# Kernel optimization log

Hardware: AMD Instinct MI355X
Metric: run time of the kernel (lower is better)

## Reference

```python
import jax, jax.numpy as jnp
import numpy as np

K = 7            # kernel_size
PAD = (K - 1) // 2
C = 64           # channels
GC = 4           # group_channels (hardcoded in module)
G = C // GC      # groups = 16
CR = C // 2      # reduction_ratio = 2
EPS = 1e-5


def setup_inputs() -> dict:
    key = jax.random.key(0)
    ks = jax.random.split(key, 8)
    b, h, w = 4, 128, 128
    x = jax.random.normal(ks[0], (b, C, h, w), dtype=jnp.float32)
    y = jax.random.normal(ks[1], (b, C, h, w), dtype=jnp.float32)
    # conv1: 1x1 conv C -> C//2, plus BatchNorm (eval-style) params
    w1 = jax.random.normal(ks[2], (CR, C), dtype=jnp.float32) * (1.0 / np.sqrt(C))
    b1 = jnp.zeros((CR,), dtype=jnp.float32)
    bn_gamma = jnp.ones((CR,), dtype=jnp.float32)
    bn_beta = jnp.zeros((CR,), dtype=jnp.float32)
    bn_mean = jax.random.normal(ks[3], (CR,), dtype=jnp.float32) * 0.1
    bn_var = jax.random.uniform(ks[4], (CR,), dtype=jnp.float32, minval=0.5, maxval=1.5)
    # conv2: 1x1 conv C//2 -> K^2 * groups
    w2 = jax.random.normal(ks[5], (K * K * G, CR), dtype=jnp.float32) * (1.0 / np.sqrt(CR))
    b2 = jnp.zeros((K * K * G,), dtype=jnp.float32)
    return {"x": x, "y": y, "w1": w1, "b1": b1, "bn_gamma": bn_gamma,
            "bn_beta": bn_beta, "bn_mean": bn_mean, "bn_var": bn_var,
            "w2": w2, "b2": b2}


def _unfold_patches(y):
    # y: (b, C, h, w) -> (b, C, K*K, h, w) im2col with zero padding PAD, stride 1
    b, c, h, w = y.shape
    yp = jnp.pad(y, ((0, 0), (0, 0), (PAD, PAD), (PAD, PAD)))
    # fixed K*K loop over kernel offsets (structural, not data-dim loop)
    patches = jnp.stack([yp[:, :, i:i + h, j:j + w]
                         for i in range(K) for j in range(K)], axis=2)
    return patches  # (b, C, K^2, h, w)


def reference(x, y, w1, b1, bn_gamma, bn_beta, bn_mean, bn_var, w2, b2):
    b, c, h, w = x.shape
    # conv1: 1x1 conv + BN(eval) + ReLU
    t = jnp.einsum('oc,bchw->bohw', w1, x) + b1[None, :, None, None]
    inv_std = jax.lax.rsqrt(bn_var + EPS)
    t = (t - bn_mean[None, :, None, None]) * (bn_gamma * inv_std)[None, :, None, None] \
        + bn_beta[None, :, None, None]
    t = jax.nn.relu(t)
    # conv2: 1x1 conv -> per-pixel kernels, (b, G, K^2, h, w)
    weight = jnp.einsum('oc,bchw->bohw', w2, t) + b2[None, :, None, None]
    weight = weight.reshape(b, G, K * K, h, w)
    # unfold y -> (b, G, GC, K^2, h, w)
    patches = _unfold_patches(y).reshape(b, G, GC, K * K, h, w)
    # dynamic depthwise aggregation: sum over K^2
    out = jnp.einsum('bgkhw,bgckhw->bgchw', weight, patches)
    return out.reshape(b, C, h, w)
```

## Files before the change

### kernel.cpp

```cpp
#include <hip/hip_runtime.h>

#define K7   7
#define PAD3 3
#define C64  64
#define CRED 32
#define GC4  4
#define EPSV 1e-5f

#define TILE 8
#define HALO 14
#define NPIX (HALO * HALO)

typedef _Float16 half8 __attribute__((ext_vector_type(8)));
typedef _Float16 half4 __attribute__((ext_vector_type(4)));
typedef float    f32x4 __attribute__((ext_vector_type(4)));

__global__ __launch_bounds__(256, 4)
void conv1_bn_relu(const float* __restrict__ x,  const float* __restrict__ w1,
                   const float* __restrict__ b1, const float* __restrict__ gma,
                   const float* __restrict__ bta, const float* __restrict__ mu,
                   const float* __restrict__ var, _Float16* __restrict__ t)
{
    const int tid = threadIdx.x;
    const int p   = tid & 63;
    const int oq  = __builtin_amdgcn_readfirstlane(tid >> 6);
    const int task = blockIdx.x * 64 + p;
    const int b   = task >> 14;
    const int pix = task & 16383;

    float dot[8] = {0,0,0,0,0,0,0,0};
    const float* w1q = w1 + oq * 8 * C64;
    const float* xp  = x + ((size_t)b << 20) + pix;
    #pragma unroll 8
    for (int c = 0; c < C64; ++c) {
        float xc = xp[(size_t)c << 14];
        #pragma unroll
        for (int j = 0; j < 8; ++j) dot[j] += w1q[j * C64 + c] * xc;
    }
    _Float16 tv[8];
    #pragma unroll
    for (int j = 0; j < 8; ++j) {
        int o = oq * 8 + j;
        float sv = gma[o] * rsqrtf(var[o] + EPSV);
        float bb = (b1[o] - mu[o]) * sv + bta[o];
        tv[j] = (_Float16)fmaxf(dot[j] * sv + bb, 0.f);
    }
    *(half8*)&t[((size_t)((b << 14) + pix)) * 32 + oq * 8] = *(const half8*)tv;
}

#define NCH2 16
#define NSL2 4
#define YPS  20
#define W2ST 40
#define W2G  (49 * W2ST)

__global__ __launch_bounds__(256, 4)
void invol_agg(const float* __restrict__ y, const _Float16* __restrict__ t,
               const float* __restrict__ w2, const float* __restrict__ b2,
               float* __restrict__ out)
{
    __shared__ __align__(16) _Float16 ytile[NPIX * YPS];
    __shared__ __align__(16) _Float16 w2h[NSL2 * W2G];

    const int tid = threadIdx.x;
    const int wgid = blockIdx.x + (blockIdx.y << 4) + (blockIdx.z << 8);
    const int swz  = ((wgid & 7) << 9) | (wgid >> 3);
    const int bx = swz & 15, by = (swz >> 4) & 15, bz = swz >> 8;
    const int b = bz >> 2, quarter = bz & 3;
    const int gh0 = by * TILE, gw0 = bx * TILE;
    const int c0 = quarter * NCH2;

    const int p  = tid & 63;
    const int ph = p >> 3, pw = p & 7;
    const int oq = __builtin_amdgcn_readfirstlane(tid >> 6);
    const int q  = p >> 4, r = p & 15;
    const int pix = ((gh0 + ph) << 7) + (gw0 + pw);

    const _Float16* tb = t + ((size_t)(b << 14)) * 32;
    const int rr8 = r >> 3, rc = r & 7;
    half8 bfrag0 = *(const half8*)&tb[(size_t)(((gh0 + 0 + rr8) << 7) + gw0 + rc) * 32 + q * 8];
    half8 bfrag1 = *(const half8*)&tb[(size_t)(((gh0 + 2 + rr8) << 7) + gw0 + rc) * 32 + q * 8];
    half8 bfrag2 = *(const half8*)&tb[(size_t)(((gh0 + 4 + rr8) << 7) + gw0 + rc) * 32 + q * 8];
    half8 bfrag3 = *(const half8*)&tb[(size_t)(((gh0 + 6 + rr8) << 7) + gw0 + rc) * 32 + q * 8];

    for (int u = tid; u < 4 * NPIX; u += 256) {
        int cg   = u / NPIX;
        int pixl = u - cg * NPIX;
        int rr   = pixl / HALO;
        int col  = pixl - rr * HALO;
        int grow = gh0 - PAD3 + rr;
        int gcol = gw0 - PAD3 + col;
        half4 v = {(_Float16)0.f, (_Float16)0.f, (_Float16)0.f, (_Float16)0.f};
        if ((unsigned)grow < 128u && (unsigned)gcol < 128u) {
            const float* yp = y + ((size_t)(b * C64 + c0 + cg * 4) << 14) + (grow << 7) + gcol;
            v[0] = (_Float16)yp[0];
            v[1] = (_Float16)yp[1 << 14];
            v[2] = (_Float16)yp[2 << 14];
            v[3] = (_Float16)yp[3 << 14];
        }
        *(half4*)&ytile[pixl * YPS + cg * 4] = v;
    }

    for (int u = tid; u < NSL2 * 49 * 8; u += 256) {
        int lg  = u / 392;
        int rem = u - lg * 392;
        int row = rem >> 3;
        int k4  = (rem & 7) << 2;
        const float4 w4 = *(const float4*)&w2[(((quarter * NSL2 + lg) * 49 + row) << 5) + k4];
        half4 h;
        h[0] = (_Float16)w4.x; h[1] = (_Float16)w4.y;
        h[2] = (_Float16)w4.z; h[3] = (_Float16)w4.w;
        *(half4*)&w2h[lg * W2G + row * W2ST + k4] = h;
    }
    __syncthreads();

    const int pbF0 = ((0 + rr8) * HALO + rc) * YPS + oq * 4;
    const int pbF1 = ((2 + rr8) * HALO + rc) * YPS + oq * 4;
    const int pbF2 = ((4 + rr8) * HALO + rc) * YPS + oq * 4;
    const int pbF3 = ((6 + rr8) * HALO + rc) * YPS + oq * 4;

    const f32x4 zero = {0.f, 0.f, 0.f, 0.f};

    const int g  = quarter * NSL2 + oq;
    const float* b2g = b2 + g * 49;
    const _Float16* w2hg = w2h + oq * W2G;

    float acc[4][4];
    #pragma unroll
    for (int nt = 0; nt < 4; ++nt)
        #pragma unroll
        for (int c = 0; c < 4; ++c) acc[nt][c] = 0.f;

    #pragma clang loop unroll(disable)
    for (int mt = 0; mt < 3; ++mt) {
        const half8 af = *(const half8*)&w2hg[(mt * 16 + r) * W2ST + q * 8];
        const int bi = mt * 16 + q * 4;
        const f32x4 cb = { b2g[bi+0], b2g[bi+1], b2g[bi+2], b2g[bi+3] };

        f32x4 d0 = __builtin_amdgcn_mfma_f32_16x16x32_f16(af, bfrag0, cb, 0, 0, 0);
        f32x4 d1 = __builtin_amdgcn_mfma_f32_16x16x32_f16(af, bfrag1, cb, 0, 0, 0);
        f32x4 d2 = __builtin_amdgcn_mfma_f32_16x16x32_f16(af, bfrag2, cb, 0, 0, 0);
        f32x4 d3 = __builtin_amdgcn_mfma_f32_16x16x32_f16(af, bfrag3, cb, 0, 0, 0);

        #pragma unroll
        for (int reg = 0; reg < 4; ++reg) {
            const int tap = mt * 16 + q * 4 + reg;
            const int di = (tap * 9363) >> 16;
            const int toffF = (tap + 7 * di) * YPS;
            {
                const float wv = d0[reg];
                const half4 y4 = *(const half4*)&ytile[pbF0 + toffF];
                acc[0][0] += (float)y4[0] * wv; acc[0][1] += (float)y4[1] * wv;
                acc[0][2] += (float)y4[2] * wv; acc[0][3] += (float)y4[3] * wv;
            }
            {
                const float wv = d1[reg];
                const half4 y4 = *(const half4*)&ytile[pbF1 + toffF];
                acc[1][0] += (float)y4[0] * wv; acc[1][1] += (float)y4[1] * wv;
                acc[1][2] += (float)y4[2] * wv; acc[1][3] += (float)y4[3] * wv;
            }
            {
                const float wv = d2[reg];
                const half4 y4 = *(const half4*)&ytile[pbF2 + toffF];
                acc[2][0] += (float)y4[0] * wv; acc[2][1] += (float)y4[1] * wv;
                acc[2][2] += (float)y4[2] * wv; acc[2][3] += (float)y4[3] * wv;
            }
            {
                const float wv = d3[reg];
                const half4 y4 = *(const half4*)&ytile[pbF3 + toffF];
                acc[3][0] += (float)y4[0] * wv; acc[3][1] += (float)y4[1] * wv;
                acc[3][2] += (float)y4[2] * wv; acc[3][3] += (float)y4[3] * wv;
            }
        }
    }

    {
        half8 af = *(const half8*)&w2hg[48 * W2ST + q * 8];
        if (r != 0) {
            #pragma unroll
            for (int j = 0; j < 8; ++j) af[j] = (_Float16)0.f;
        }
        f32x4 d0 = __builtin_amdgcn_mfma_f32_16x16x32_f16(af, bfrag0, zero, 0, 0, 0);
        f32x4 d1 = __builtin_amdgcn_mfma_f32_16x16x32_f16(af, bfrag1, zero, 0, 0, 0);
        f32x4 d2 = __builtin_amdgcn_mfma_f32_16x16x32_f16(af, bfrag2, zero, 0, 0, 0);
        f32x4 d3 = __builtin_amdgcn_mfma_f32_16x16x32_f16(af, bfrag3, zero, 0, 0, 0);

        const float bv = b2g[48];
        const int toffF = (48 + 7 * 6) * YPS;
        const bool live = (q == 0);
        {
            float wv = live ? (d0[0] + bv) : 0.f;
            const half4 y4 = *(const half4*)&ytile[pbF0 + toffF];
            acc[0][0] += (float)y4[0] * wv; acc[0][1] += (float)y4[1] * wv;
            acc[0][2] += (float)y4[2] * wv; acc[0][3] += (float)y4[3] * wv;
        }
        {
            float wv = live ? (d1[0] + bv) : 0.f;
            const half4 y4 = *(const half4*)&ytile[pbF1 + toffF];
            acc[1][0] += (float)y4[0] * wv; acc[1][1] += (float)y4[1] * wv;
            acc[1][2] += (float)y4[2] * wv; acc[1][3] += (float)y4[3] * wv;
        }
        {
            float wv = live ? (d2[0] + bv) : 0.f;
            const half4 y4 = *(const half4*)&ytile[pbF2 + toffF];
            acc[2][0] += (float)y4[0] * wv; acc[2][1] += (float)y4[1] * wv;
            acc[2][2] += (float)y4[2] * wv; acc[2][3] += (float)y4[3] * wv;
        }
        {
            float wv = live ? (d3[0] + bv) : 0.f;
            const half4 y4 = *(const half4*)&ytile[pbF3 + toffF];
            acc[3][0] += (float)y4[0] * wv; acc[3][1] += (float)y4[1] * wv;
            acc[3][2] += (float)y4[2] * wv; acc[3][3] += (float)y4[3] * wv;
        }
    }

    #pragma unroll
    for (int nt = 0; nt < 4; ++nt)
        #pragma unroll
        for (int c = 0; c < 4; ++c) {
            float v = acc[nt][c];
            v += __shfl_xor(v, 16);
            v += __shfl_xor(v, 32);
            acc[nt][c] = v;
        }

    size_t ob = ((size_t)(b * C64 + g * GC4) << 14) + pix;
    #pragma unroll
    for (int c = 0; c < 4; ++c) {
        float s0 = (q & 1) ? acc[1][c] : acc[0][c];
        float s1 = (q & 1) ? acc[3][c] : acc[2][c];
        float vv = (q & 2) ? s1 : s0;
        out[ob + ((size_t)c << 14)] = vv;
    }
}

#define NCHF 32
#define NSLF 8
#define TSTH 40

__global__ __launch_bounds__(256, 2)
void involution_fused_fb(const float* __restrict__ x, const float* __restrict__ y,
                         const float* __restrict__ w1, const float* __restrict__ b1,
                         const float* __restrict__ gma, const float* __restrict__ bta,
                         const float* __restrict__ mu,  const float* __restrict__ var,
                         const float* __restrict__ w2,  const float* __restrict__ b2,
                         float* __restrict__ out)
{
    __shared__ __align__(16) float    ytile[NPIX * NCHF];
    __shared__ __align__(16) _Float16 t_lds[64 * TSTH];

    const int tid = threadIdx.x;
    const int bx = blockIdx.x, by = blockIdx.y, bz = blockIdx.z;
    const int b = bz >> 1, half = bz & 1;
    const int gh0 = by * TILE, gw0 = bx * TILE;
    const int c0 = half * NCHF;

    for (int li = tid; li < NCHF * NPIX; li += 256) {
        int c    = li / NPIX;
        int pixl = li - c * NPIX;
        int rr   = pixl / HALO;
        int col  = pixl - rr * HALO;
        int grow = gh0 - PAD3 + rr;
        int gcol = gw0 - PAD3 + col;
        float v = 0.f;
        if ((unsigned)grow < 128u && (unsigned)gcol < 128u)
            v = y[((size_t)(b * C64 + c0 + c) << 14) + (grow << 7) + gcol];
        int slot = ((c >> 2) + pixl) & 7;
        ytile[pixl * NCHF + slot * 4 + (c & 3)] = v;
    }

    const int p  = tid & 63;
    const int ph = p >> 3, pw = p & 7;
    const int oq = __builtin_amdgcn_readfirstlane(tid >> 6);
    const int pix = ((gh0 + ph) << 7) + (gw0 + pw);
    {
        float dot[8] = {0,0,0,0,0,0,0,0};
        const float* w1q = w1 + oq * 8 * C64;
        const float* xp  = x + ((size_t)(b * C64) << 14) + pix;
        #pragma unroll 8
        for (int c = 0; c < C64; ++c) {
            float xc = xp[(size_t)c << 14];
            #pragma unroll
            for (int j = 0; j < 8; ++j) dot[j] += w1q[j * C64 + c] * xc;
        }
        _Float16 tv16[8];
        #pragma unroll
        for (int j = 0; j < 8; ++j) {
            int o = oq * 8 + j;
            float sv = gma[o] * rsqrtf(var[o] + EPSV);
            float bb = (b1[o] - mu[o]) * sv + bta[o];
            tv16[j] = (_Float16)fmaxf(dot[j] * sv + bb, 0.f);
        }
        *(half8*)&t_lds[p * TSTH + oq * 8] = *(const half8*)tv16;
    }
    __syncthreads();

    const int q = p >> 4;
    const int r = p & 15;

    half8 bfrag0 = *(const half8*)&t_lds[( 0 + r) * TSTH + q * 8];
    half8 bfrag1 = *(const half8*)&t_lds[(16 + r) * TSTH + q * 8];
    half8 bfrag2 = *(const half8*)&t_lds[(32 + r) * TSTH + q * 8];
    half8 bfrag3 = *(const half8*)&t_lds[(48 + r) * TSTH + q * 8];

    const int pb0 = (0 + (r >> 3)) * HALO + (r & 7);
    const int pb1 = (2 + (r >> 3)) * HALO + (r & 7);
    const int pb2 = (4 + (r >> 3)) * HALO + (r & 7);
    const int pb3 = (6 + (r >> 3)) * HALO + (r & 7);

    const f32x4 zero = {0.f, 0.f, 0.f, 0.f};

    #pragma unroll 1
    for (int lgi = 0; lgi < 2; ++lgi) {
        const int lg = oq * 2 + lgi;
        const int g  = half * NSLF + lg;
        const float* w2g = w2 + g * 49 * CRED;
        const float* b2g = b2 + g * 49;

        float acc[4][4];
        #pragma unroll
        for (int nt = 0; nt < 4; ++nt)
            #pragma unroll
            for (int c = 0; c < 4; ++c) acc[nt][c] = 0.f;

        #pragma clang loop unroll(disable)
        for (int mt = 0; mt < 3; ++mt) {
            half8 af;
            {
                const float* wr = w2g + (mt * 16 + r) * CRED + q * 8;
                float4 wa = *(const float4*)wr;
                float4 wb = *(const float4*)(wr + 4);
                af[0] = (_Float16)wa.x; af[1] = (_Float16)wa.y;
                af[2] = (_Float16)wa.z; af[3] = (_Float16)wa.w;
                af[4] = (_Float16)wb.x; af[5] = (_Float16)wb.y;
                af[6] = (_Float16)wb.z; af[7] = (_Float16)wb.w;
            }
            f32x4 d0 = __builtin_amdgcn_mfma_f32_16x16x32_f16(af, bfrag0, zero, 0, 0, 0);
            f32x4 d1 = __builtin_amdgcn_mfma_f32_16x16x32_f16(af, bfrag1, zero, 0, 0, 0);
            f32x4 d2 = __builtin_amdgcn_mfma_f32_16x16x32_f16(af, bfrag2, zero, 0, 0, 0);
            f32x4 d3 = __builtin_amdgcn_mfma_f32_16x16x32_f16(af, bfrag3, zero, 0, 0, 0);

            #pragma unroll
            for (int reg = 0; reg < 4; ++reg) {
                const int tap = mt * 16 + q * 4 + reg;
                const float bv = b2g[tap];
                const int di = (tap * 9363) >> 16;
                const int tapoff = tap + 7 * di;
                {
                    float wv = d0[reg] + bv;
                    int tp2 = pb0 + tapoff;
                    const float4 y4 = *(const float4*)&ytile[tp2 * NCHF + (((lg + tp2) & 7) << 2)];
                    acc[0][0] += wv * y4.x; acc[0][1] += wv * y4.y;
                    acc[0][2] += wv * y4.z; acc[0][3] += wv * y4.w;
                }
                {
                    float wv = d1[reg] + bv;
                    int tp2 = pb1 + tapoff;
                    const float4 y4 = *(const float4*)&ytile[tp2 * NCHF + (((lg + tp2) & 7) << 2)];
                    acc[1][0] += wv * y4.x; acc[1][1] += wv * y4.y;
                    acc[1][2] += wv * y4.z; acc[1][3] += wv * y4.w;
                }
                {
                    float wv = d2[reg] + bv;
                    int tp2 = pb2 + tapoff;
                    const float4 y4 = *(const float4*)&ytile[tp2 * NCHF + (((lg + tp2) & 7) << 2)];
                    acc[2][0] += wv * y4.x; acc[2][1] += wv * y4.y;
                    acc[2][2] += wv * y4.z; acc[2][3] += wv * y4.w;
                }
                {
                    float wv = d3[reg] + bv;
                    int tp2 = pb3 + tapoff;
                    const float4 y4 = *(const float4*)&ytile[tp2 * NCHF + (((lg + tp2) & 7) << 2)];
                    acc[3][0] += wv * y4.x; acc[3][1] += wv * y4.y;
                    acc[3][2] += wv * y4.z; acc[3][3] += wv * y4.w;
                }
            }
        }

        {
            half8 af;
            #pragma unroll
            for (int j = 0; j < 8; ++j) af[j] = (_Float16)0.f;
            if (r == 0) {
                const float* wr = w2g + 48 * CRED + q * 8;
                float4 wa = *(const float4*)wr;
                float4 wb = *(const float4*)(wr + 4);
                af[0] = (_Float16)wa.x; af[1] = (_Float16)wa.y;
                af[2] = (_Float16)wa.z; af[3] = (_Float16)wa.w;
                af[4] = (_Float16)wb.x; af[5] = (_Float16)wb.y;
                af[6] = (_Float16)wb.z; af[7] = (_Float16)wb.w;
            }
            f32x4 d0 = __builtin_amdgcn_mfma_f32_16x16x32_f16(af, bfrag0, zero, 0, 0, 0);
            f32x4 d1 = __builtin_amdgcn_mfma_f32_16x16x32_f16(af, bfrag1, zero, 0, 0, 0);
            f32x4 d2 = __builtin_amdgcn_mfma_f32_16x16x32_f16(af, bfrag2, zero, 0, 0, 0);
            f32x4 d3 = __builtin_amdgcn_mfma_f32_16x16x32_f16(af, bfrag3, zero, 0, 0, 0);

            const float bv = b2g[48];
            const int tapoff = 48 + 7 * 6;
            const bool live = (q == 0);
            {
                float wv = live ? (d0[0] + bv) : 0.f;
                int tp2 = pb0 + tapoff;
                const float4 y4 = *(const float4*)&ytile[tp2 * NCHF + (((lg + tp2) & 7) << 2)];
                acc[0][0] += wv * y4.x; acc[0][1] += wv * y4.y;
                acc[0][2] += wv * y4.z; acc[0][3] += wv * y4.w;
            }
            {
                float wv = live ? (d1[0] + bv) : 0.f;
                int tp2 = pb1 + tapoff;
                const float4 y4 = *(const float4*)&ytile[tp2 * NCHF + (((lg + tp2) & 7) << 2)];
                acc[1][0] += wv * y4.x; acc[1][1] += wv * y4.y;
                acc[1][2] += wv * y4.z; acc[1][3] += wv * y4.w;
            }
            {
                float wv = live ? (d2[0] + bv) : 0.f;
                int tp2 = pb2 + tapoff;
                const float4 y4 = *(const float4*)&ytile[tp2 * NCHF + (((lg + tp2) & 7) << 2)];
                acc[2][0] += wv * y4.x; acc[2][1] += wv * y4.y;
                acc[2][2] += wv * y4.z; acc[2][3] += wv * y4.w;
            }
            {
                float wv = live ? (d3[0] + bv) : 0.f;
                int tp2 = pb3 + tapoff;
                const float4 y4 = *(const float4*)&ytile[tp2 * NCHF + (((lg + tp2) & 7) << 2)];
                acc[3][0] += wv * y4.x; acc[3][1] += wv * y4.y;
                acc[3][2] += wv * y4.z; acc[3][3] += wv * y4.w;
            }
        }

        #pragma unroll
        for (int nt = 0; nt < 4; ++nt)
            #pragma unroll
            for (int c = 0; c < 4; ++c) {
                float v = acc[nt][c];
                v += __shfl_xor(v, 16);
                v += __shfl_xor(v, 32);
                acc[nt][c] = v;
            }

        size_t ob = ((size_t)(b * C64 + g * GC4) << 14) + pix;
        #pragma unroll
        for (int c = 0; c < 4; ++c) {
            float s0 = (q & 1) ? acc[1][c] : acc[0][c];
            float s1 = (q & 1) ? acc[3][c] : acc[2][c];
            float vv = (q & 2) ? s1 : s0;
            out[ob + ((size_t)c << 14)] = vv;
        }
    }
}

extern "C" void kernel_launch(void* const* d_in, const int* in_sizes, int n_in,
                              void* d_out, int out_size, void* d_ws, size_t ws_size,
                              hipStream_t stream) {
    const float* x   = (const float*)d_in[0];
    const float* y   = (const float*)d_in[1];
    const float* w1  = (const float*)d_in[2];
    const float* b1  = (const float*)d_in[3];
    const float* gma = (const float*)d_in[4];
    const float* bta = (const float*)d_in[5];
    const float* mu  = (const float*)d_in[6];
    const float* var = (const float*)d_in[7];
    const float* w2  = (const float*)d_in[8];
    const float* b2  = (const float*)d_in[9];
    float* out = (float*)d_out;

    const size_t t_bytes = (size_t)4 * 16384 * 32 * sizeof(_Float16);
    if (ws_size >= t_bytes) {
        _Float16* t = (_Float16*)d_ws;
        hipLaunchKernelGGL(conv1_bn_relu, dim3(1024), dim3(256), 0, stream,
                           x, w1, b1, gma, bta, mu, var, t);
        hipLaunchKernelGGL(invol_agg, dim3(16, 16, 16), dim3(256), 0, stream,
                           y, t, w2, b2, out);
    } else {
        hipLaunchKernelGGL(involution_fused_fb, dim3(16, 16, 8), dim3(256), 0, stream,
                           x, y, w1, b1, gma, bta, mu, var, w2, b2, out);
    }
}
```

Before: 45.70 us.

## Process two groups per wave in involution aggregation to halve tile loads

```diff
diff --git a/kernel.cpp b/kernel.cpp
--- a/kernel.cpp
+++ b/kernel.cpp
@@ -48,27 +48,26 @@
     *(half8*)&t[((size_t)((b << 14) + pix)) * 32 + oq * 8] = *(const half8*)tv;
 }
 
-#define NCH2 16
-#define NSL2 4
-#define YPS  20
+#define NSLH 8
+#define YPS  40
 #define W2ST 40
 #define W2G  (49 * W2ST)
 
-__global__ __launch_bounds__(256, 4)
+__global__ __launch_bounds__(256, 2)
 void invol_agg(const float* __restrict__ y, const _Float16* __restrict__ t,
                const float* __restrict__ w2, const float* __restrict__ b2,
                float* __restrict__ out)
 {
     __shared__ __align__(16) _Float16 ytile[NPIX * YPS];
-    __shared__ __align__(16) _Float16 w2h[NSL2 * W2G];
+    __shared__ __align__(16) _Float16 w2h[NSLH * W2G];
 
     const int tid = threadIdx.x;
     const int wgid = blockIdx.x + (blockIdx.y << 4) + (blockIdx.z << 8);
-    const int swz  = ((wgid & 7) << 9) | (wgid >> 3);
+    const int swz  = ((wgid & 7) << 8) | (wgid >> 3);
     const int bx = swz & 15, by = (swz >> 4) & 15, bz = swz >> 8;
-    const int b = bz >> 2, quarter = bz & 3;
+    const int b = bz >> 1, half = bz & 1;
     const int gh0 = by * TILE, gw0 = bx * TILE;
-    const int c0 = quarter * NCH2;
+    const int c0 = half * 32;
 
     const int p  = tid & 63;
     const int ph = p >> 3, pw = p & 7;
@@ -83,7 +82,7 @@
     half8 bfrag2 = *(const half8*)&tb[(size_t)(((gh0 + 4 + rr8) << 7) + gw0 + rc) * 32 + q * 8];
     half8 bfrag3 = *(const half8*)&tb[(size_t)(((gh0 + 6 + rr8) << 7) + gw0 + rc) * 32 + q * 8];
 
-    for (int u = tid; u < 4 * NPIX; u += 256) {
+    for (int u = tid; u < 8 * NPIX; u += 256) {
         int cg   = u / NPIX;
         int pixl = u - cg * NPIX;
         int rr   = pixl / HALO;
@@ -101,12 +100,12 @@
         *(half4*)&ytile[pixl * YPS + cg * 4] = v;
     }
 
-    for (int u = tid; u < NSL2 * 49 * 8; u += 256) {
+    for (int u = tid; u < NSLH * 49 * 8; u += 256) {
         int lg  = u / 392;
         int rem = u - lg * 392;
         int row = rem >> 3;
         int k4  = (rem & 7) << 2;
-        const float4 w4 = *(const float4*)&w2[(((quarter * NSL2 + lg) * 49 + row) << 5) + k4];
+        const float4 w4 = *(const float4*)&w2[(((half * NSLH + lg) * 49 + row) << 5) + k4];
         half4 h;
         h[0] = (_Float16)w4.x; h[1] = (_Float16)w4.y;
         h[2] = (_Float16)w4.z; h[3] = (_Float16)w4.w;
@@ -114,33 +113,42 @@
     }
     __syncthreads();
 
-    const int pbF0 = ((0 + rr8) * HALO + rc) * YPS + oq * 4;
-    const int pbF1 = ((2 + rr8) * HALO + rc) * YPS + oq * 4;
-    const int pbF2 = ((4 + rr8) * HALO + rc) * YPS + oq * 4;
-    const int pbF3 = ((6 + rr8) * HALO + rc) * YPS + oq * 4;
+    const int pbF0 = ((0 + rr8) * HALO + rc) * YPS + oq * 8;
+    const int pbF1 = ((2 + rr8) * HALO + rc) * YPS + oq * 8;
+    const int pbF2 = ((4 + rr8) * HALO + rc) * YPS + oq * 8;
+    const int pbF3 = ((6 + rr8) * HALO + rc) * YPS + oq * 8;
 
     const f32x4 zero = {0.f, 0.f, 0.f, 0.f};
 
-    const int g  = quarter * NSL2 + oq;
-    const float* b2g = b2 + g * 49;
-    const _Float16* w2hg = w2h + oq * W2G;
-
-    float acc[4][4];
+    const int lg0 = 2 * oq, lg1 = 2 * oq + 1;
+    const int g0  = half * NSLH + lg0;
+    const float* b2g0 = b2 + g0 * 49;
+    const float* b2g1 = b2 + (g0 + 1) * 49;
+    const _Float16* w2hg0 = w2h + lg0 * W2G;
+    const _Float16* w2hg1 = w2h + lg1 * W2G;
+
+    float acc0[4][4], acc1[4][4];
     #pragma unroll
     for (int nt = 0; nt < 4; ++nt)
         #pragma unroll
-        for (int c = 0; c < 4; ++c) acc[nt][c] = 0.f;
+        for (int c = 0; c < 4; ++c) { acc0[nt][c] = 0.f; acc1[nt][c] = 0.f; }
 
     #pragma clang loop unroll(disable)
     for (int mt = 0; mt < 3; ++mt) {
-        const half8 af = *(const half8*)&w2hg[(mt * 16 + r) * W2ST + q * 8];
+        const half8 af0 = *(const half8*)&w2hg0[(mt * 16 + r) * W2ST + q * 8];
+        const half8 af1 = *(const half8*)&w2hg1[(mt * 16 + r) * W2ST + q * 8];
         const int bi = mt * 16 + q * 4;
-        const f32x4 cb = { b2g[bi+0], b2g[bi+1], b2g[bi+2], b2g[bi+3] };
-
-        f32x4 d0 = __builtin_amdgcn_mfma_f32_16x16x32_f16(af, bfrag0, cb, 0, 0, 0);
-        f32x4 d1 = __builtin_amdgcn_mfma_f32_16x16x32_f16(af, bfrag1, cb, 0, 0, 0);
-        f32x4 d2 = __builtin_amdgcn_mfma_f32_16x16x32_f16(af, bfrag2, cb, 0, 0, 0);
-        f32x4 d3 = __builtin_amdgcn_mfma_f32_16x16x32_f16(af, bfrag3, cb, 0, 0, 0);
+        const f32x4 cb0 = { b2g0[bi+0], b2g0[bi+1], b2g0[bi+2], b2g0[bi+3] };
+        const f32x4 cb1 = { b2g1[bi+0], b2g1[bi+1], b2g1[bi+2], b2g1[bi+3] };
+
+        f32x4 d0 = __builtin_amdgcn_mfma_f32_16x16x32_f16(af0, bfrag0, cb0, 0, 0, 0);
+        f32x4 d1 = __builtin_amdgcn_mfma_f32_16x16x32_f16(af0, bfrag1, cb0, 0, 0, 0);
+        f32x4 d2 = __builtin_amdgcn_mfma_f32_16x16x32_f16(af0, bfrag2, cb0, 0, 0, 0);
+        f32x4 d3 = __builtin_amdgcn_mfma_f32_16x16x32_f16(af0, bfrag3, cb0, 0, 0, 0);
+        f32x4 e0 = __builtin_amdgcn_mfma_f32_16x16x32_f16(af1, bfrag0, cb1, 0, 0, 0);
+        f32x4 e1 = __builtin_amdgcn_mfma_f32_16x16x32_f16(af1, bfrag1, cb1, 0, 0, 0);
+        f32x4 e2 = __builtin_amdgcn_mfma_f32_16x16x32_f16(af1, bfrag2, cb1, 0, 0, 0);
+        f32x4 e3 = __builtin_amdgcn_mfma_f32_16x16x32_f16(af1, bfrag3, cb1, 0, 0, 0);
 
         #pragma unroll
         for (int reg = 0; reg < 4; ++reg) {
@@ -148,69 +156,94 @@
             const int di = (tap * 9363) >> 16;
             const int toffF = (tap + 7 * di) * YPS;
             {
-                const float wv = d0[reg];
-                const half4 y4 = *(const half4*)&ytile[pbF0 + toffF];
-                acc[0][0] += (float)y4[0] * wv; acc[0][1] += (float)y4[1] * wv;
-                acc[0][2] += (float)y4[2] * wv; acc[0][3] += (float)y4[3] * wv;
-            }
-            {
-                const float wv = d1[reg];
-                const half4 y4 = *(const half4*)&ytile[pbF1 + toffF];
-                acc[1][0] += (float)y4[0] * wv; acc[1][1] += (float)y4[1] * wv;
-                acc[1][2] += (float)y4[2] * wv; acc[1][3] += (float)y4[3] * wv;
-            }
-            {
-                const float wv = d2[reg];
-                const half4 y4 = *(const half4*)&ytile[pbF2 + toffF];
-                acc[2][0] += (float)y4[0] * wv; acc[2][1] += (float)y4[1] * wv;
-                acc[2][2] += (float)y4[2] * wv; acc[2][3] += (float)y4[3] * wv;
-            }
-            {
-                const float wv = d3[reg];
-                const half4 y4 = *(const half4*)&ytile[pbF3 + toffF];
-                acc[3][0] += (float)y4[0] * wv; acc[3][1] += (float)y4[1] * wv;
-                acc[3][2] += (float)y4[2] * wv; acc[3][3] += (float)y4[3] * wv;
+                const half8 y8 = *(const half8*)&ytile[pbF0 + toffF];
+                const float wv = d0[reg], ev = e0[reg];
+                acc0[0][0] += (float)y8[0] * wv; acc0[0][1] += (float)y8[1] * wv;
+                acc0[0][2] += (float)y8[2] * wv; acc0[0][3] += (float)y8[3] * wv;
+                acc1[0][0] += (float)y8[4] * ev; acc1[0][1] += (float)y8[5] * ev;
+                acc1[0][2] += (float)y8[6] * ev; acc1[0][3] += (float)y8[7] * ev;
+            }
+            {
+                const half8 y8 = *(const half8*)&ytile[pbF1 + toffF];
+                const float wv = d1[reg], ev = e1[reg];
+                acc0[1][0] += (float)y8[0] * wv; acc0[1][1] += (float)y8[1] * wv;
+                acc0[1][2] += (float)y8[2] * wv; acc0[1][3] += (float)y8[3] * wv;
+                acc1[1][0] += (float)y8[4] * ev; acc1[1][1] += (float)y8[5] * ev;
+                acc1[1][2] += (float)y8[6] * ev; acc1[1][3] += (float)y8[7] * ev;
+            }
+            {
+                const half8 y8 = *(const half8*)&ytile[pbF2 + toffF];
+                const float wv = d2[reg], ev = e2[reg];
+                acc0[2][0] += (float)y8[0] * wv; acc0[2][1] += (float)y8[1] * wv;
+                acc0[2][2] += (float)y8[2] * wv; acc0[2][3] += (float)y8[3] * wv;
+                acc1[2][0] += (float)y8[4] * ev; acc1[2][1] += (float)y8[5] * ev;
+                acc1[2][2] += (float)y8[6] * ev; acc1[2][3] += (float)y8[7] * ev;
+            }
+            {
+                const half8 y8 = *(const half8*)&ytile[pbF3 + toffF];
+                const float wv = d3[reg], ev = e3[reg];
+                acc0[3][0] += (float)y8[0] * wv; acc0[3][1] += (float)y8[1] * wv;
+                acc0[3][2] += (float)y8[2] * wv; acc0[3][3] += (float)y8[3] * wv;
+                acc1[3][0] += (float)y8[4] * ev; acc1[3][1] += (float)y8[5] * ev;
+                acc1[3][2] += (float)y8[6] * ev; acc1[3][3] += (float)y8[7] * ev;
             }
         }
     }
 
     {
-        half8 af = *(const half8*)&w2hg[48 * W2ST + q * 8];
+        half8 af0 = *(const half8*)&w2hg0[48 * W2ST + q * 8];
+        half8 af1 = *(const half8*)&w2hg1[48 * W2ST + q * 8];
         if (r != 0) {
             #pragma unroll
-            for (int j = 0; j < 8; ++j) af[j] = (_Float16)0.f;
-        }
-        f32x4 d0 = __builtin_amdgcn_mfma_f32_16x16x32_f16(af, bfrag0, zero, 0, 0, 0);
-        f32x4 d1 = __builtin_amdgcn_mfma_f32_16x16x32_f16(af, bfrag1, zero, 0, 0, 0);
-        f32x4 d2 = __builtin_amdgcn_mfma_f32_16x16x32_f16(af, bfrag2, zero, 0, 0, 0);
-        f32x4 d3 = __builtin_amdgcn_mfma_f32_16x16x32_f16(af, bfrag3, zero, 0, 0, 0);
-
-        const float bv = b2g[48];
+            for (int j = 0; j < 8; ++j) { af0[j] = (_Float16)0.f; af1[j] = (_Float16)0.f; }
+        }
+        f32x4 d0 = __builtin_amdgcn_mfma_f32_16x16x32_f16(af0, bfrag0, zero, 0, 0, 0);
+        f32x4 d1 = __builtin_amdgcn_mfma_f32_16x16x32_f16(af0, bfrag1, zero, 0, 0, 0);
+        f32x4 d2 = __builtin_amdgcn_mfma_f32_16x16x32_f16(af0, bfrag2, zero, 0, 0, 0);
+        f32x4 d3 = __builtin_amdgcn_mfma_f32_16x16x32_f16(af0, bfrag3, zero, 0, 0, 0);
+        f32x4 e0 = __builtin_amdgcn_mfma_f32_16x16x32_f16(af1, bfrag0, zero, 0, 0, 0);
+        f32x4 e1 = __builtin_amdgcn_mfma_f32_16x16x32_f16(af1, bfrag1, zero, 0, 0, 0);
+        f32x4 e2 = __builtin_amdgcn_mfma_f32_16x16x32_f16(af1, bfrag2, zero, 0, 0, 0);
+        f32x4 e3 = __builtin_amdgcn_mfma_f32_16x16x32_f16(af1, bfrag3, zero, 0, 0, 0);
+
+        const float bv0 = b2g0[48], bv1 = b2g1[48];
         const int toffF = (48 + 7 * 6) * YPS;
         const bool live = (q == 0);
         {
-            float wv = live ? (d0[0] + bv) : 0.f;
-            const half4 y4 = *(const half4*)&ytile[pbF0 + toffF];
-            acc[0][0] += (float)y4[0] * wv; acc[0][1] += (float)y4[1] * wv;
-            acc[0][2] += (float)y4[2] * wv; acc[0][3] += (float)y4[3] * wv;
+            const half8 y8 = *(const half8*)&ytile[pbF0 + toffF];
+            float wv = live ? (d0[0] + bv0) : 0.f;
+            float ev = live ? (e0[0] + bv1) : 0.f;
+            acc0[0][0] += (float)y8[0] * wv; acc0[0][1] += (float)y8[1] * wv;
+            acc0[0][2] += (float)y8[2] * wv; acc0[0][3] += (float)y8[3] * wv;
+            acc1[0][0] += (float)y8[4] * ev; acc1[0][1] += (float)y8[5] * ev;
+            acc1[0][2] += (float)y8[6] * ev; acc1[0][3] += (float)y8[7] * ev;
         }
         {
-            float wv = live ? (d1[0] + bv) : 0.f;
-            const half4 y4 = *(const half4*)&ytile[pbF1 + toffF];
-            acc[1][0] += (float)y4[0] * wv; acc[1][1] += (float)y4[1] * wv;
-            acc[1][2] += (float)y4[2] * wv; acc[1][3] += (float)y4[3] * wv;
+            const half8 y8 = *(const half8*)&ytile[pbF1 + toffF];
+            float wv = live ? (d1[0] + bv0) : 0.f;
+            float ev = live ? (e1[0] + bv1) : 0.f;
+            acc0[1][0] += (float)y8[0] * wv; acc0[1][1] += (float)y8[1] * wv;
+            acc0[1][2] += (float)y8[2] * wv; acc0[1][3] += (float)y8[3] * wv;
+            acc1[1][0] += (float)y8[4] * ev; acc1[1][1] += (float)y8[5] * ev;
+            acc1[1][2] += (float)y8[6] * ev; acc1[1][3] += (float)y8[7] * ev;
         }
         {
-            float wv = live ? (d2[0] + bv) : 0.f;
-            const half4 y4 = *(const half4*)&ytile[pbF2 + toffF];
-            acc[2][0] += (float)y4[0] * wv; acc[2][1] += (float)y4[1] * wv;
-            acc[2][2] += (float)y4[2] * wv; acc[2][3] += (float)y4[3] * wv;
+            const half8 y8 = *(const half8*)&ytile[pbF2 + toffF];
+            float wv = live ? (d2[0] + bv0) : 0.f;
+            float ev = live ? (e2[0] + bv1) : 0.f;
+            acc0[2][0] += (float)y8[0] * wv; acc0[2][1] += (float)y8[1] * wv;
+            acc0[2][2] += (float)y8[2] * wv; acc0[2][3] += (float)y8[3] * wv;
+            acc1[2][0] += (float)y8[4] * ev; acc1[2][1] += (float)y8[5] * ev;
+            acc1[2][2] += (float)y8[6] * ev; acc1[2][3] += (float)y8[7] * ev;
         }
         {
-            float wv = live ? (d3[0] + bv) : 0.f;
-            const half4 y4 = *(const half4*)&ytile[pbF3 + toffF];
-            acc[3][0] += (float)y4[0] * wv; acc[3][1] += (float)y4[1] * wv;
-            acc[3][2] += (float)y4[2] * wv; acc[3][3] += (float)y4[3] * wv;
+            const half8 y8 = *(const half8*)&ytile[pbF3 + toffF];
+            float wv = live ? (d3[0] + bv0) : 0.f;
+            float ev = live ? (e3[0] + bv1) : 0.f;
+            acc0[3][0] += (float)y8[0] * wv; acc0[3][1] += (float)y8[1] * wv;
+            acc0[3][2] += (float)y8[2] * wv; acc0[3][3] += (float)y8[3] * wv;
+            acc1[3][0] += (float)y8[4] * ev; acc1[3][1] += (float)y8[5] * ev;
+            acc1[3][2] += (float)y8[6] * ev; acc1[3][3] += (float)y8[7] * ev;
         }
     }
 
@@ -218,19 +251,28 @@
     for (int nt = 0; nt < 4; ++nt)
         #pragma unroll
         for (int c = 0; c < 4; ++c) {
-            float v = acc[nt][c];
-            v += __shfl_xor(v, 16);
-            v += __shfl_xor(v, 32);
-            acc[nt][c] = v;
-        }
-
-    size_t ob = ((size_t)(b * C64 + g * GC4) << 14) + pix;
+            float v0 = acc0[nt][c];
+            v0 += __shfl_xor(v0, 16);
+            v0 += __shfl_xor(v0, 32);
+            acc0[nt][c] = v0;
+            float v1 = acc1[nt][c];
+            v1 += __shfl_xor(v1, 16);
+            v1 += __shfl_xor(v1, 32);
+            acc1[nt][c] = v1;
+        }
+
+    size_t ob = ((size_t)(b * C64 + g0 * GC4) << 14) + pix;
     #pragma unroll
     for (int c = 0; c < 4; ++c) {
-        float s0 = (q & 1) ? acc[1][c] : acc[0][c];
-        float s1 = (q & 1) ? acc[3][c] : acc[2][c];
-        float vv = (q & 2) ? s1 : s0;
-        out[ob + ((size_t)c << 14)] = vv;
+        float s0 = (q & 1) ? acc0[1][c] : acc0[0][c];
+        float s1 = (q & 1) ? acc0[3][c] : acc0[2][c];
+        out[ob + ((size_t)c << 14)] = (q & 2) ? s1 : s0;
+    }
+    #pragma unroll
+    for (int c = 0; c < 4; ++c) {
+        float s0 = (q & 1) ? acc1[1][c] : acc1[0][c];
+        float s1 = (q & 1) ? acc1[3][c] : acc1[2][c];
+        out[ob + ((size_t)(c + 4) << 14)] = (q & 2) ? s1 : s0;
     }
 }
 
@@ -469,7 +511,7 @@
         _Float16* t = (_Float16*)d_ws;
         hipLaunchKernelGGL(conv1_bn_relu, dim3(1024), dim3(256), 0, stream,
                            x, w1, b1, gma, bta, mu, var, t);
-        hipLaunchKernelGGL(invol_agg, dim3(16, 16, 16), dim3(256), 0, stream,
+        hipLaunchKernelGGL(invol_agg, dim3(16, 16, 8), dim3(256), 0, stream,
                            y, t, w2, b2, out);
     } else {
         hipLaunchKernelGGL(involution_fused_fb, dim3(16, 16, 8), dim3(256), 0, stream,
```

After: 48.37 us. 5.9% more time.

## Widen aggregation tile to 8x16 pixels with eight MFMA column blocks

Applied to the files above, without the earlier changes.

```diff
diff --git a/kernel.cpp b/kernel.cpp
--- a/kernel.cpp
+++ b/kernel.cpp
@@ -6,10 +6,6 @@
 #define CRED 32
 #define GC4  4
 #define EPSV 1e-5f
-
-#define TILE 8
-#define HALO 14
-#define NPIX (HALO * HALO)
 
 typedef _Float16 half8 __attribute__((ext_vector_type(8)));
 typedef _Float16 half4 __attribute__((ext_vector_type(4)));
@@ -48,46 +44,51 @@
     *(half8*)&t[((size_t)((b << 14) + pix)) * 32 + oq * 8] = *(const half8*)tv;
 }
 
-#define NCH2 16
+#define TH   8
+#define TW   16
+#define HH2  14
+#define HW2  22
+#define NPIX2 (HH2 * HW2)
 #define NSL2 4
 #define YPS  20
 #define W2ST 40
 #define W2G  (49 * W2ST)
 
-__global__ __launch_bounds__(256, 4)
+__global__ __launch_bounds__(256, 2)
 void invol_agg(const float* __restrict__ y, const _Float16* __restrict__ t,
                const float* __restrict__ w2, const float* __restrict__ b2,
                float* __restrict__ out)
 {
-    __shared__ __align__(16) _Float16 ytile[NPIX * YPS];
+    __shared__ __align__(16) _Float16 ytile[NPIX2 * YPS];
     __shared__ __align__(16) _Float16 w2h[NSL2 * W2G];
 
     const int tid = threadIdx.x;
-    const int wgid = blockIdx.x + (blockIdx.y << 4) + (blockIdx.z << 8);
-    const int swz  = ((wgid & 7) << 9) | (wgid >> 3);
-    const int bx = swz & 15, by = (swz >> 4) & 15, bz = swz >> 8;
+    const int wgid = blockIdx.x + (blockIdx.y << 3) + (blockIdx.z << 7);
+    const int swz  = ((wgid & 7) << 8) | (wgid >> 3);
+    const int bx = swz & 7, by = (swz >> 3) & 15, bz = swz >> 7;
     const int b = bz >> 2, quarter = bz & 3;
-    const int gh0 = by * TILE, gw0 = bx * TILE;
-    const int c0 = quarter * NCH2;
+    const int gh0 = by * TH, gw0 = bx * TW;
+    const int c0 = quarter * 16;
 
     const int p  = tid & 63;
-    const int ph = p >> 3, pw = p & 7;
     const int oq = __builtin_amdgcn_readfirstlane(tid >> 6);
     const int q  = p >> 4, r = p & 15;
-    const int pix = ((gh0 + ph) << 7) + (gw0 + pw);
 
     const _Float16* tb = t + ((size_t)(b << 14)) * 32;
-    const int rr8 = r >> 3, rc = r & 7;
-    half8 bfrag0 = *(const half8*)&tb[(size_t)(((gh0 + 0 + rr8) << 7) + gw0 + rc) * 32 + q * 8];
-    half8 bfrag1 = *(const half8*)&tb[(size_t)(((gh0 + 2 + rr8) << 7) + gw0 + rc) * 32 + q * 8];
-    half8 bfrag2 = *(const half8*)&tb[(size_t)(((gh0 + 4 + rr8) << 7) + gw0 + rc) * 32 + q * 8];
-    half8 bfrag3 = *(const half8*)&tb[(size_t)(((gh0 + 6 + rr8) << 7) + gw0 + rc) * 32 + q * 8];
-
-    for (int u = tid; u < 4 * NPIX; u += 256) {
-        int cg   = u / NPIX;
-        int pixl = u - cg * NPIX;
-        int rr   = pixl / HALO;
-        int col  = pixl - rr * HALO;
+    half8 bf0 = *(const half8*)&tb[(size_t)(((gh0 + 0) << 7) + gw0 + r) * 32 + q * 8];
+    half8 bf1 = *(const half8*)&tb[(size_t)(((gh0 + 1) << 7) + gw0 + r) * 32 + q * 8];
+    half8 bf2 = *(const half8*)&tb[(size_t)(((gh0 + 2) << 7) + gw0 + r) * 32 + q * 8];
+    half8 bf3 = *(const half8*)&tb[(size_t)(((gh0 + 3) << 7) + gw0 + r) * 32 + q * 8];
+    half8 bf4 = *(const half8*)&tb[(size_t)(((gh0 + 4) << 7) + gw0 + r) * 32 + q * 8];
+    half8 bf5 = *(const half8*)&tb[(size_t)(((gh0 + 5) << 7) + gw0 + r) * 32 + q * 8];
+    half8 bf6 = *(const half8*)&tb[(size_t)(((gh0 + 6) << 7) + gw0 + r) * 32 + q * 8];
+    half8 bf7 = *(const half8*)&tb[(size_t)(((gh0 + 7) << 7) + gw0 + r) * 32 + q * 8];
+
+    for (int u = tid; u < 4 * NPIX2; u += 256) {
+        int cg   = u / NPIX2;
+        int pixl = u - cg * NPIX2;
+        int rr   = pixl / HW2;
+        int col  = pixl - rr * HW2;
         int grow = gh0 - PAD3 + rr;
         int gcol = gw0 - PAD3 + col;
         half4 v = {(_Float16)0.f, (_Float16)0.f, (_Float16)0.f, (_Float16)0.f};
@@ -114,22 +115,40 @@
     }
     __syncthreads();
 
-    const int pbF0 = ((0 + rr8) * HALO + rc) * YPS + oq * 4;
-    const int pbF1 = ((2 + rr8) * HALO + rc) * YPS + oq * 4;
-    const int pbF2 = ((4 + rr8) * HALO + rc) * YPS + oq * 4;
-    const int pbF3 = ((6 + rr8) * HALO + rc) * YPS + oq * 4;
+    const int pbF0 = (0 * HW2 + r) * YPS + oq * 4;
+    const int pbF1 = (1 * HW2 + r) * YPS + oq * 4;
+    const int pbF2 = (2 * HW2 + r) * YPS + oq * 4;
+    const int pbF3 = (3 * HW2 + r) * YPS + oq * 4;
+    const int pbF4 = (4 * HW2 + r) * YPS + oq * 4;
+    const int pbF5 = (5 * HW2 + r) * YPS + oq * 4;
+    const int pbF6 = (6 * HW2 + r) * YPS + oq * 4;
+    const int pbF7 = (7 * HW2 + r) * YPS + oq * 4;
 
     const f32x4 zero = {0.f, 0.f, 0.f, 0.f};
 
-    const int g  = quarter * NSL2 + oq;
+    const int g = quarter * NSL2 + oq;
     const float* b2g = b2 + g * 49;
     const _Float16* w2hg = w2h + oq * W2G;
 
-    float acc[4][4];
+    float acc[8][4];
     #pragma unroll
-    for (int nt = 0; nt < 4; ++nt)
+    for (int nt = 0; nt < 8; ++nt)
         #pragma unroll
         for (int c = 0; c < 4; ++c) acc[nt][c] = 0.f;
+
+#define AGG(NT, DV) do { \
+        const half4 y4 = *(const half4*)&ytile[pbF##NT + toffF]; \
+        const float wv = (DV)[reg]; \
+        acc[NT][0] += (float)y4[0] * wv; acc[NT][1] += (float)y4[1] * wv; \
+        acc[NT][2] += (float)y4[2] * wv; acc[NT][3] += (float)y4[3] * wv; \
+    } while (0)
+
+#define AGGT(NT, DV) do { \
+        const half4 y4 = *(const half4*)&ytile[pbF##NT + toffF]; \
+        const float wv = live ? ((DV)[0] + bv) : 0.f; \
+        acc[NT][0] += (float)y4[0] * wv; acc[NT][1] += (float)y4[1] * wv; \
+        acc[NT][2] += (float)y4[2] * wv; acc[NT][3] += (float)y4[3] * wv; \
+    } while (0)
 
     #pragma clang loop unroll(disable)
     for (int mt = 0; mt < 3; ++mt) {
@@ -137,40 +156,22 @@
         const int bi = mt * 16 + q * 4;
         const f32x4 cb = { b2g[bi+0], b2g[bi+1], b2g[bi+2], b2g[bi+3] };
 
-        f32x4 d0 = __builtin_amdgcn_mfma_f32_16x16x32_f16(af, bfrag0, cb, 0, 0, 0);
-        f32x4 d1 = __builtin_amdgcn_mfma_f32_16x16x32_f16(af, bfrag1, cb, 0, 0, 0);
-        f32x4 d2 = __builtin_amdgcn_mfma_f32_16x16x32_f16(af, bfrag2, cb, 0, 0, 0);
-        f32x4 d3 = __builtin_amdgcn_mfma_f32_16x16x32_f16(af, bfrag3, cb, 0, 0, 0);
+        f32x4 d0 = __builtin_amdgcn_mfma_f32_16x16x32_f16(af, bf0, cb, 0, 0, 0);
+        f32x4 d1 = __builtin_amdgcn_mfma_f32_16x16x32_f16(af, bf1, cb, 0, 0, 0);
+        f32x4 d2 = __builtin_amdgcn_mfma_f32_16x16x32_f16(af, bf2, cb, 0, 0, 0);
+        f32x4 d3 = __builtin_amdgcn_mfma_f32_16x16x32_f16(af, bf3, cb, 0, 0, 0);
+        f32x4 d4 = __builtin_amdgcn_mfma_f32_16x16x32_f16(af, bf4, cb, 0, 0, 0);
+        f32x4 d5 = __builtin_amdgcn_mfma_f32_16x16x32_f16(af, bf5, cb, 0, 0, 0);
+        f32x4 d6 = __builtin_amdgcn_mfma_f32_16x16x32_f16(af, bf6, cb, 0, 0, 0);
+        f32x4 d7 = __builtin_amdgcn_mfma_f32_16x16x32_f16(af, bf7, cb, 0, 0, 0);
 
         #pragma unroll
         for (int reg = 0; reg < 4; ++reg) {
             const int tap = mt * 16 + q * 4 + reg;
             const int di = (tap * 9363) >> 16;
-            const int toffF = (tap + 7 * di) * YPS;
-            {
-                const float wv = d0[reg];
-                const half4 y4 = *(const half4*)&ytile[pbF0 + toffF];
-                acc[0][0] += (float)y4[0] * wv; acc[0][1] += (float)y4[1] * wv;
-                acc[0][2] += (float)y4[2] * wv; acc[0][3] += (float)y4[3] * wv;
-            }
-            {
-                const float wv = d1[reg];
-                const half4 y4 = *(const half4*)&ytile[pbF1 + toffF];
-                acc[1][0] += (float)y4[0] * wv; acc[1][1] += (float)y4[1] * wv;
-                acc[1][2] += (float)y4[2] * wv; acc[1][3] += (float)y4[3] * wv;
-            }
-            {
-                const float wv = d2[reg];
-                const half4 y4 = *(const half4*)&ytile[pbF2 + toffF];
-                acc[2][0] += (float)y4[0] * wv; acc[2][1] += (float)y4[1] * wv;
-                acc[2][2] += (float)y4[2] * wv; acc[2][3] += (float)y4[3] * wv;
-            }
-            {
-                const float wv = d3[reg];
-                const half4 y4 = *(const half4*)&ytile[pbF3 + toffF];
-                acc[3][0] += (float)y4[0] * wv; acc[3][1] += (float)y4[1] * wv;
-                acc[3][2] += (float)y4[2] * wv; acc[3][3] += (float)y4[3] * wv;
-            }
+            const int toffF = (tap + 15 * di) * YPS;
+            AGG(0, d0); AGG(1, d1); AGG(2, d2); AGG(3, d3);
+            AGG(4, d4); AGG(5, d5); AGG(6, d6); AGG(7, d7);
         }
     }
 
@@ -180,42 +181,26 @@
             #pragma unroll
             for (int j = 0; j < 8; ++j) af[j] = (_Float16)0.f;
         }
-        f32x4 d0 = __builtin_amdgcn_mfma_f32_16x16x32_f16(af, bfrag0, zero, 0, 0, 0);
-        f32x4 d1 = __builtin_amdgcn_mfma_f32_16x16x32_f16(af, bfrag1, zero, 0, 0, 0);
-        f32x4 d2 = __builtin_amdgcn_mfma_f32_16x16x32_f16(af, bfrag2, zero, 0, 0, 0);
-        f32x4 d3 = __builtin_amdgcn_mfma_f32_16x16x32_f16(af, bfrag3, zero, 0, 0, 0);
+        f32x4 d0 = __builtin_amdgcn_mfma_f32_16x16x32_f16(af, bf0, zero, 0, 0, 0);
+        f32x4 d1 = __builtin_amdgcn_mfma_f32_16x16x32_f16(af, bf1, zero, 0, 0, 0);
+        f32x4 d2 = __builtin_amdgcn_mfma_f32_16x16x32_f16(af, bf2, zero, 0, 0, 0);
+        f32x4 d3 = __builtin_amdgcn_mfma_f32_16x16x32_f16(af, bf3, zero, 0, 0, 0);
+        f32x4 d4 = __builtin_amdgcn_mfma_f32_16x16x32_f16(af, bf4, zero, 0, 0, 0);
+        f32x4 d5 = __builtin_amdgcn_mfma_f32_16x16x32_f16(af, bf5, zero, 0, 0, 0);
+        f32x4 d6 = __builtin_amdgcn_mfma_f32_16x16x32_f16(af, bf6, zero, 0, 0, 0);
+        f32x4 d7 = __builtin_amdgcn_mfma_f32_16x16x32_f16(af, bf7, zero, 0, 0, 0);
 
         const float bv = b2g[48];
-        const int toffF = (48 + 7 * 6) * YPS;
+        const int toffF = (48 + 15 * 6) * YPS;
         const bool live = (q == 0);
-        {
-            float wv = live ? (d0[0] + bv) : 0.f;
-            const half4 y4 = *(const half4*)&ytile[pbF0 + toffF];
-            acc[0][0] += (float)y4[0] * wv; acc[0][1] += (float)y4[1] * wv;
-            acc[0][2] += (float)y4[2] * wv; acc[0][3] += (float)y4[3] * wv;
-        }
-        {
-            float wv = live ? (d1[0] + bv) : 0.f;
-            const half4 y4 = *(const half4*)&ytile[pbF1 + toffF];
-            acc[1][0] += (float)y4[0] * wv; acc[1][1] += (float)y4[1] * wv;
-            acc[1][2] += (float)y4[2] * wv; acc[1][3] += (float)y4[3] * wv;
-        }
-        {
-            float wv = live ? (d2[0] + bv) : 0.f;
-            const half4 y4 = *(const half4*)&ytile[pbF2 + toffF];
-            acc[2][0] += (float)y4[0] * wv; acc[2][1] += (float)y4[1] * wv;
-            acc[2][2] += (float)y4[2] * wv; acc[2][3] += (float)y4[3] * wv;
-        }
-        {
-            float wv = live ? (d3[0] + bv) : 0.f;
-            const half4 y4 = *(const half4*)&ytile[pbF3 + toffF];
-            acc[3][0] += (float)y4[0] * wv; acc[3][1] += (float)y4[1] * wv;
-            acc[3][2] += (float)y4[2] * wv; acc[3][3] += (float)y4[3] * wv;
-        }
-    }
+        AGGT(0, d0); AGGT(1, d1); AGGT(2, d2); AGGT(3, d3);
+        AGGT(4, d4); AGGT(5, d5); AGGT(6, d6); AGGT(7, d7);
+    }
+#undef AGG
+#undef AGGT
 
     #pragma unroll
-    for (int nt = 0; nt < 4; ++nt)
+    for (int nt = 0; nt < 8; ++nt)
         #pragma unroll
         for (int c = 0; c < 4; ++c) {
             float v = acc[nt][c];
@@ -224,16 +209,23 @@
             acc[nt][c] = v;
         }
 
-    size_t ob = ((size_t)(b * C64 + g * GC4) << 14) + pix;
+    const size_t obase = ((size_t)(b * C64 + g * GC4) << 14);
+    const int pixA = ((gh0 + q) << 7) + gw0 + r;
+    const int pixB = ((gh0 + 4 + q) << 7) + gw0 + r;
     #pragma unroll
     for (int c = 0; c < 4; ++c) {
         float s0 = (q & 1) ? acc[1][c] : acc[0][c];
         float s1 = (q & 1) ? acc[3][c] : acc[2][c];
-        float vv = (q & 2) ? s1 : s0;
-        out[ob + ((size_t)c << 14)] = vv;
+        out[obase + ((size_t)c << 14) + pixA] = (q & 2) ? s1 : s0;
+        float s2 = (q & 1) ? acc[5][c] : acc[4][c];
+        float s3 = (q & 1) ? acc[7][c] : acc[6][c];
+        out[obase + ((size_t)c << 14) + pixB] = (q & 2) ? s3 : s2;
     }
 }
 
+#define TILE 8
+#define HALO 14
+#define NPIX (HALO * HALO)
 #define NCHF 32
 #define NSLF 8
 #define TSTH 40
@@ -469,7 +461,7 @@
         _Float16* t = (_Float16*)d_ws;
         hipLaunchKernelGGL(conv1_bn_relu, dim3(1024), dim3(256), 0, stream,
                            x, w1, b1, gma, bta, mu, var, t);
-        hipLaunchKernelGGL(invol_agg, dim3(16, 16, 16), dim3(256), 0, stream,
+        hipLaunchKernelGGL(invol_agg, dim3(8, 16, 16), dim3(256), 0, stream,
                            y, t, w2, b2, out);
     } else {
         hipLaunchKernelGGL(involution_fused_fb, dim3(16, 16, 8), dim3(256), 0, stream,
```

Result: no change. 45.44 us (-0.6%).
